# Kernel tuning notes

Hardware: AMD Instinct MI355X
Metric: run time of the kernel (lower is better)

The kernel has to match this reference:

```python
import jax, jax.numpy as jnp
import numpy as np


def _lstm_dir(xs, Wih, Whh, bih, bhh, reverse):
    # xs: [T, B, E]; torch LSTM gate order i, f, g, o
    B = xs.shape[1]
    H = Whh.shape[1]
    h0 = jnp.zeros((B, H), xs.dtype)
    c0 = jnp.zeros((B, H), xs.dtype)

    def step(carry, xt):
        h, c = carry
        g = xt @ Wih.T + h @ Whh.T + (bih + bhh)
        i, f, gg, o = jnp.split(g, 4, axis=-1)
        i = jax.nn.sigmoid(i)
        f = jax.nn.sigmoid(f)
        gg = jnp.tanh(gg)
        o = jax.nn.sigmoid(o)
        c_new = f * c + i * gg
        h_new = o * jnp.tanh(c_new)
        return (h_new, c_new), h_new

    _, hs = jax.lax.scan(step, (h0, c0), xs, reverse=reverse)
    return hs  # [T, B, H] time-aligned


def _forward(x, edge_index, emb_table, Wih_f, Whh_f, bih_f, bhh_f,
             Wih_b, Whh_b, bih_b, bhh_b, label_emb, ggc_weight,
             gru_Wih, gru_Whh, gru_bih, gru_bhh, proj_W, proj_b):
    # --- embedding (dropout is identity in eval) ---
    emb = emb_table[x]                       # [B, T, E]
    xs = jnp.transpose(emb, (1, 0, 2))       # [T, B, E]
    hf = _lstm_dir(xs, Wih_f, Whh_f, bih_f, bhh_f, reverse=False)
    hb = _lstm_dir(xs, Wih_b, Whh_b, bih_b, bhh_b, reverse=True)
    c = jnp.concatenate([hf, hb], axis=-1)   # [T, B, 2H]
    c = jnp.transpose(c, (1, 0, 2))          # [B, T, 2H]

    # --- label cosine similarity, summed over tokens ---
    eps = 1e-8
    cn = c / jnp.maximum(jnp.linalg.norm(c, axis=-1, keepdims=True), eps)
    ln = label_emb / jnp.maximum(jnp.linalg.norm(label_emb, axis=-1, keepdims=True), eps)
    ls = jnp.einsum('btd,ld->bl', cn, ln)    # [B, C] (sum over t folded in)

    # --- GatedGraphConv, 2 layers, aggr='add', edge_weight=None ---
    src, dst = edge_index[0], edge_index[1]
    N = ls.shape[0]
    h = ls
    for i in range(ggc_weight.shape[0]):
        m = h @ ggc_weight[i]                            # [N, C]
        m = jax.ops.segment_sum(m[src], dst, num_segments=N)  # gather + scatter-add
        # torch GRUCell: gates r, z, n
        gi = m @ gru_Wih.T + gru_bih
        gh = h @ gru_Whh.T + gru_bhh
        ir, iz, inn = jnp.split(gi, 3, axis=-1)
        hr, hz, hn = jnp.split(gh, 3, axis=-1)
        r = jax.nn.sigmoid(ir + hr)
        z = jax.nn.sigmoid(iz + hz)
        n = jnp.tanh(inn + r * hn)
        h = (1.0 - z) * n + z * h

    return h @ proj_W.T + proj_b             # [B, C]


def setup_inputs() -> dict:
    key = jax.random.key(0)
    ks = jax.random.split(key, 20)
    V, E, B, T, C, NE = 50000, 300, 2048, 64, 1024, 65536
    H = E
    s = 0.05
    inp = {
        'x': jax.random.randint(ks[0], (B, T), 0, V),
        'edge_index': jax.random.randint(ks[1], (2, NE), 0, B),
        'emb_table': jax.random.normal(ks[2], (V, E)) * s,
        'Wih_f': jax.random.normal(ks[3], (4 * H, E)) * s,
        'Whh_f': jax.random.normal(ks[4], (4 * H, H)) * s,
        'bih_f': jnp.zeros((4 * H,)),
        'bhh_f': jnp.zeros((4 * H,)),
        'Wih_b': jax.random.normal(ks[5], (4 * H, E)) * s,
        'Whh_b': jax.random.normal(ks[6], (4 * H, H)) * s,
        'bih_b': jnp.zeros((4 * H,)),
        'bhh_b': jnp.zeros((4 * H,)),
        'label_emb': jax.random.normal(ks[7], (C, 2 * H)) * s,
        'ggc_weight': jax.random.normal(ks[8], (2, C, C)) * (1.0 / np.sqrt(C)),
        'gru_Wih': jax.random.normal(ks[9], (3 * C, C)) * (1.0 / np.sqrt(C)),
        'gru_Whh': jax.random.normal(ks[10], (3 * C, C)) * (1.0 / np.sqrt(C)),
        'gru_bih': jnp.zeros((3 * C,)),
        'gru_bhh': jnp.zeros((3 * C,)),
        'proj_W': jax.random.normal(ks[11], (C, C)) * (1.0 / np.sqrt(C)),
        'proj_b': jnp.zeros((C,)),
    }
    return inp


def reference(x, edge_index, emb_table, Wih_f, Whh_f, bih_f, bhh_f,
              Wih_b, Whh_b, bih_b, bhh_b, label_emb, ggc_weight,
              gru_Wih, gru_Whh, gru_bih, gru_bhh, proj_W, proj_b):
    return _forward(x, edge_index, emb_table, Wih_f, Whh_f, bih_f, bhh_f,
                    Wih_b, Whh_b, bih_b, bhh_b, label_emb, ggc_weight,
                    gru_Wih, gru_Whh, gru_bih, gru_bhh, proj_W, proj_b)
```

## Files before the change

### kernel.cpp

```cpp
#include <hip/hip_runtime.h>
#include <hip/hip_bf16.h>
#include <stdint.h>

typedef __hip_bfloat16 bf16;
typedef __attribute__((ext_vector_type(8))) short frag16;
typedef __attribute__((ext_vector_type(4))) float f32x4;

#define B_ 2048
#define T_ 64
#define E_ 300
#define H_ 300
#define C_ 1024
#define V_ 50000
#define NE_ 65536
#define HP 320
#define KC 640
#define NP 1280

static __device__ __forceinline__ float sigf(float x) {
  x = fminf(fmaxf(x, -30.f), 30.f);
  return 1.f / (1.f + __expf(-x));
}
static __device__ __forceinline__ float tanhfast(float x) {
  x = fminf(fmaxf(x, -15.f), 15.f);
  float e = __expf(2.f * x);
  return (e - 1.f) / (e + 1.f);
}
static __device__ __forceinline__ float ldraw(const void* p, size_t i, int isb) {
  return isb ? __bfloat162float(((const bf16*)p)[i]) : ((const float*)p)[i];
}
static __device__ __forceinline__ short b2s(bf16 b) {
  short s; __builtin_memcpy(&s, &b, 2); return s;
}
static __device__ __forceinline__ short4 f4tob4(float4 v) {
  return make_short4(b2s(__float2bfloat16(v.x)), b2s(__float2bfloat16(v.y)),
                     b2s(__float2bfloat16(v.z)), b2s(__float2bfloat16(v.w)));
}

static __device__ __forceinline__ void g2l16(const void* g, void* l) {
  __builtin_amdgcn_global_load_lds(
      (const __attribute__((address_space(1))) void*)(uintptr_t)g,
      (__attribute__((address_space(3))) void*)(uintptr_t)l, 16, 0, 0);
}

__global__ void detect_dtype(const unsigned short* __restrict__ e2, int* __restrict__ flag) {
  __shared__ int red[4];
  int tid = threadIdx.x;
  int ones = 0;
#pragma unroll
  for (int s = 0; s < 16; ++s) ones += (e2[2 * (tid * 16 + s)] >> 14) & 1;
  for (int off = 32; off > 0; off >>= 1) ones += __shfl_down(ones, off, 64);
  if ((tid & 63) == 0) red[tid >> 6] = ones;
  __syncthreads();
  if (tid == 0) {
    int tot = red[0] + red[1] + red[2] + red[3];
    *flag = (tot < 1024) ? 1 : 0;
  }
}

__global__ __launch_bounds__(256) void gemm_bt(
    const bf16* A, int lda, const bf16* W, int ldw, const float* bias,
    float* Cf, bf16* Cb, int ldc, int K,
    const int* __restrict__ rawp, int outmode,
    const bf16* A2, const bf16* W2, const float* bias2, float* Cf2) {
  if (blockIdx.z) { A = A2; W = W2; bias = bias2; Cf = Cf2; Cb = nullptr; }
  __shared__ __align__(16) short As[128 * 32];
  __shared__ __align__(16) short Bs[128 * 32];
  const int isb = rawp ? *rawp : 1;
  const int n0 = blockIdx.x * 128, m0 = blockIdx.y * 128;
  const int lane = threadIdx.x & 63, wv = threadIdx.x >> 6;
  const int wm = (wv & 1) * 64, wn = (wv >> 1) * 64;
  const int gr = lane >> 2;
  const int gc = (lane & 3) * 8;
  const short* pA0 = (const short*)A + (size_t)(m0 + wv * 32 + gr) * lda + gc;
  const short* pA1 = pA0 + (size_t)16 * lda;
  const short* pB0 = (const short*)W + (size_t)(n0 + wv * 32 + gr) * ldw + gc;
  const short* pB1 = pB0 + (size_t)16 * ldw;
  short* lA = As + wv * 1024;
  short* lB = Bs + wv * 1024;

  f32x4 acc[4][4];
#pragma unroll
  for (int i = 0; i < 4; ++i)
#pragma unroll
    for (int j = 0; j < 4; ++j) acc[i][j] = (f32x4){0.f, 0.f, 0.f, 0.f};

  const int krd = (lane >> 4) * 8;
  const int rsel = lane & 15;
  for (int k0 = 0; k0 < K; k0 += 32) {
    g2l16(pA0 + k0, lA);
    g2l16(pA1 + k0, lA + 512);
    g2l16(pB0 + k0, lB);
    g2l16(pB1 + k0, lB + 512);
    __syncthreads();
    frag16 af[4], bfg[4];
#pragma unroll
    for (int i = 0; i < 4; ++i) af[i] = *(const frag16*)&As[(wm + i * 16 + rsel) * 32 + krd];
#pragma unroll
    for (int i = 0; i < 4; ++i) bfg[i] = *(const frag16*)&Bs[(wn + i * 16 + rsel) * 32 + krd];
#pragma unroll
    for (int i = 0; i < 4; ++i)
#pragma unroll
      for (int j = 0; j < 4; ++j)
        acc[i][j] = __builtin_amdgcn_mfma_f32_16x16x32_bf16(af[i], bfg[j], acc[i][j], 0, 0, 0);
    __syncthreads();
  }
  const int rq = (lane >> 4) * 4, cq = lane & 15;
#pragma unroll
  for (int j = 0; j < 4; ++j) {
    int cidx = n0 + wn + j * 16 + cq;
    float bv = bias ? bias[cidx] : 0.f;
#pragma unroll
    for (int i = 0; i < 4; ++i) {
      int rbase = m0 + wm + i * 16 + rq;
#pragma unroll
      for (int r = 0; r < 4; ++r) {
        float v = acc[i][j][r] + bv;
        size_t idx = (size_t)(rbase + r) * ldc + cidx;
        if (outmode) {
          if (isb) Cb[idx] = __float2bfloat16(v);
          else Cf[idx] = v;
        } else {
          if (Cf) Cf[idx] = v;
          if (Cb) Cb[idx] = __float2bfloat16(v);
        }
      }
    }
  }
}

static __device__ __forceinline__ void normacc_row2(
    const bf16* hfA, const bf16* hbA, const bf16* hfB, const bf16* hbB,
    float* __restrict__ Spf, int b, int lane) {
  float vA[10], vB[10];
  float sA = 0.f, sB = 0.f;
#pragma unroll
  for (int s = 0; s < 10; ++s) {
    int d = lane + 64 * s;
    float a = 0.f, c = 0.f;
    if (d < 300) {
      a = __bfloat162float(hfA[d]);
      c = __bfloat162float(hfB[d]);
    } else if (d < 600) {
      a = __bfloat162float(hbA[d - 300]);
      c = __bfloat162float(hbB[d - 300]);
    }
    vA[s] = a; vB[s] = c;
    sA += a * a; sB += c * c;
  }
#pragma unroll
  for (int off = 32; off > 0; off >>= 1) {
    sA += __shfl_xor(sA, off, 64);
    sB += __shfl_xor(sB, off, 64);
  }
  float kA = 1.f / fmaxf(sqrtf(sA), 1e-8f);
  float kB = 1.f / fmaxf(sqrtf(sB), 1e-8f);
  float* dst = Spf + (size_t)b * KC;
#pragma unroll
  for (int s = 0; s < 10; ++s) {
    int d = lane + 64 * s;
    if (d < 600) dst[d] += vA[s] * kA + vB[s] * kB;
  }
}

__global__ __launch_bounds__(256) void lstm_step(
    const void* __restrict__ emb, const bf16* __restrict__ embtail,
    const int* __restrict__ x,
    const bf16* __restrict__ Wcat, const float* __restrict__ bcat,
    bf16* __restrict__ hpad, float* __restrict__ cstate,
    bf16* __restrict__ Hfst, bf16* __restrict__ Hbst, float* __restrict__ Spf,
    int s, const int* __restrict__ flagp) {
  const int pb = s & 1;
  const int lane = threadIdx.x & 63, wv = threadIdx.x >> 6;

  if (blockIdx.z == 2) {
    if (s >= 33) {
      int bid = blockIdx.x + gridDim.x * blockIdx.y;
      const bf16* hinf = hpad + (size_t)pb * B_ * HP;
      const bf16* hinb = hpad + (size_t)(2 + pb) * B_ * HP;
      const int t1 = s - 1, t2 = 64 - s;
#pragma unroll
      for (int rep = 0; rep < 2; ++rep) {
        int b = bid * 4 + wv + 1280 * rep;
        if (b < B_)
          normacc_row2(hinf + (size_t)b * HP,
                       Hbst + ((size_t)(t1 - 32) * B_ + b) * H_,
                       Hfst + ((size_t)t2 * B_ + b) * H_,
                       hinb + (size_t)b * HP, Spf, b, lane);
      }
    }
    return;
  }

  __shared__ __align__(16) char smem[16384];
  short* As = (short*)smem;
  short* Bs = (short*)(smem + 4096);
  float* epi = (float*)smem;

  const int dir = blockIdx.z;
  const int tt = dir ? (T_ - 1 - s) : s;
  const int isb = *flagp;
  const bf16* hin = hpad + (size_t)(dir * 2 + pb) * B_ * HP;
  const bf16* Wd = Wcat + (size_t)dir * NP * KC;
  bf16* hout = hpad + (size_t)(dir * 2 + (1 - pb)) * B_ * HP;
  float* cs = cstate + (size_t)dir * B_ * HP;
  const int n0 = blockIdx.x * 128, m0 = blockIdx.y * 64;
  const int wm = (wv & 1) * 32, wn = (wv >> 1) * 64;
  const int gr = lane >> 2;
  const int gc = (lane & 3) * 8;
  const int arow = m0 + wv * 16 + gr;
  const int tok = x[arow * T_ + tt];
  const short* es = (const short*)emb;
  const float* ef = (const float*)emb;
  const short* px = es + (size_t)tok * E_ + gc;
  const short* ptail = (const short*)embtail + (size_t)tok * 32 + gc;
  const short* ph = (const short*)hin + (size_t)arow * HP + gc;
  const short* pB0 = (const short*)Wd + (size_t)(n0 + wv * 32 + gr) * KC + gc;
  const short* pB1 = pB0 + (size_t)16 * KC;
  short* lA = As + wv * 512;
  short* lB = Bs + wv * 1024;

  f32x4 acc[2][4];
#pragma unroll
  for (int i = 0; i < 2; ++i)
#pragma unroll
    for (int j = 0; j < 4; ++j) acc[i][j] = (f32x4){0.f, 0.f, 0.f, 0.f};

  const int rsel = lane & 15, krd = (lane >> 4) * 8;
  for (int kk = 0; kk < KC / 32; ++kk) {
    const int k0 = kk * 32;
    if (k0 < HP) {
      if (isb) {
        g2l16(k0 == 288 ? ptail : (px + k0), lA);
      } else {
        int c0 = k0 + gc;
        float4 fa = (c0 < E_) ? *(const float4*)(ef + (size_t)tok * E_ + c0)
                              : make_float4(0.f, 0.f, 0.f, 0.f);
        float4 fb = (c0 + 4 < E_) ? *(const float4*)(ef + (size_t)tok * E_ + c0 + 4)
                                  : make_float4(0.f, 0.f, 0.f, 0.f);
        short* d = As + (wv * 16 + gr) * 32 + gc;
        *(short4*)d = f4tob4(fa);
        *(short4*)(d + 4) = f4tob4(fb);
      }
    } else {
      g2l16(ph + (k0 - HP), lA);
    }
    g2l16(pB0 + k0, lB);
    g2l16(pB1 + k0, lB + 512);
    __syncthreads();
    frag16 af[2], bfg[4];
#pragma unroll
    for (int i = 0; i < 2; ++i) af[i] = *(const frag16*)&As[(wm + i * 16 + rsel) * 32 + krd];
#pragma unroll
    for (int j = 0; j < 4; ++j) bfg[j] = *(const frag16*)&Bs[(wn + j * 16 + rsel) * 32 + krd];
#pragma unroll
    for (int i = 0; i < 2; ++i)
#pragma unroll
      for (int j = 0; j < 4; ++j)
        acc[i][j] = __builtin_amdgcn_mfma_f32_16x16x32_bf16(af[i], bfg[j], acc[i][j], 0, 0, 0);
    __syncthreads();
  }

  const int rq = (lane >> 4) * 4, cq = lane & 15;
#pragma unroll
  for (int p = 0; p < 2; ++p) {
    if (wn == p * 64) {
#pragma unroll
      for (int j = 0; j < 4; ++j) {
        int cl = j * 16 + cq;
        float bv = bcat[dir * NP + n0 + p * 64 + cl];
#pragma unroll
        for (int i = 0; i < 2; ++i) {
          int rl = wm + i * 16 + rq;
#pragma unroll
          for (int r = 0; r < 4; ++r) epi[(rl + r) * 64 + cl] = acc[i][j][r] + bv;
        }
      }
    }
    __syncthreads();
    int jbase = (n0 + p * 64) >> 2;
    for (int it = threadIdx.x; it < 64 * 16; it += 256) {
      int rl = it >> 4, jl = it & 15;
      int jg = jbase + jl;
      if (jg < H_) {
        const float* row = epi + rl * 64 + jl * 4;
        float iv = sigf(row[0]);
        float fv = sigf(row[1]);
        float gv = tanhfast(row[2]);
        float ov = sigf(row[3]);
        int b = m0 + rl;
        float c = fv * cs[(size_t)b * HP + jg] + iv * gv;
        float h = ov * tanhfast(c);
        cs[(size_t)b * HP + jg] = c;
        bf16 hb = __float2bfloat16(h);
        hout[(size_t)b * HP + jg] = hb;
        if (dir) {
          if (tt >= 32) Hbst[((size_t)(tt - 32) * B_ + b) * H_ + jg] = hb;
        } else if (tt < 32) {
          Hfst[((size_t)tt * B_ + b) * H_ + jg] = hb;
        }
      }
    }
    __syncthreads();
  }
}

__global__ __launch_bounds__(256) void normacc_fin(const bf16* __restrict__ hpad,
                                                   const bf16* __restrict__ Hfst,
                                                   const bf16* __restrict__ Hbst,
                                                   float* __restrict__ Spf) {
  int b = blockIdx.x * 4 + (threadIdx.x >> 6);
  int lane = threadIdx.x & 63;
  normacc_row2(hpad + (size_t)b * HP,
               Hbst + ((size_t)31 * B_ + b) * H_,
               Hfst + (size_t)b * H_,
               hpad + (size_t)2 * B_ * HP + (size_t)b * HP, Spf, b, lane);
}

__global__ void prep_all(const void* __restrict__ Wih_f, const void* __restrict__ Whh_f,
                         const void* __restrict__ bih_f, const void* __restrict__ bhh_f,
                         const void* __restrict__ Wih_b, const void* __restrict__ Whh_b,
                         const void* __restrict__ bih_b, const void* __restrict__ bhh_b,
                         const void* __restrict__ label, const void* __restrict__ ggcw,
                         const void* __restrict__ emb,
                         bf16* __restrict__ Wcat, float* __restrict__ bcat,
                         bf16* __restrict__ lnp, bf16* __restrict__ ggct,
                         bf16* __restrict__ embtail,
                         const int* __restrict__ flagp) {
  const int isb = *flagp;
  if (blockIdx.x < 1024) {
    int l = blockIdx.x, tid = threadIdx.x;
    __shared__ float red[4];
    float v[3];
    float ss = 0.f;
#pragma unroll
    for (int s = 0; s < 3; ++s) {
      int d = tid + 256 * s;
      v[s] = (d < 600) ? ldraw(label, (size_t)l * 600 + d, isb) : 0.f;
      ss += v[s] * v[s];
    }
    for (int off = 32; off > 0; off >>= 1) ss += __shfl_down(ss, off, 64);
    if ((tid & 63) == 0) red[tid >> 6] = ss;
    __syncthreads();
    float scale = 1.f / fmaxf(sqrtf(red[0] + red[1] + red[2] + red[3]), 1e-8f);
#pragma unroll
    for (int s = 0; s < 3; ++s) {
      int d = tid + 256 * s;
      if (d < KC) lnp[(size_t)l * KC + d] = __float2bfloat16(v[s] * scale);
    }
    return;
  }
  int i = (blockIdx.x - 1024) * 256 + threadIdx.x;
  if (i < 2 * NP * KC) {
    int k = i % KC;
    int n = (i / KC) % NP;
    int dir = i / (KC * NP);
    int j = n >> 2, q = n & 3;
    const void* Wih = dir ? Wih_b : Wih_f;
    const void* Whh = dir ? Whh_b : Whh_f;
    float v = 0.f;
    if (j < H_) {
      int row = q * H_ + j;
      if (k < E_) v = ldraw(Wih, (size_t)row * E_ + k, isb);
      else if (k >= HP && k < HP + H_) v = ldraw(Whh, (size_t)row * H_ + (k - HP), isb);
    }
    Wcat[i] = __float2bfloat16(v);
    if (k == 0) {
      const void* bih = dir ? bih_b : bih_f;
      const void* bhh = dir ? bhh_b : bhh_f;
      bcat[dir * NP + n] =
          (j < H_) ? (ldraw(bih, q * H_ + j, isb) + ldraw(bhh, q * H_ + j, isb)) : 0.f;
    }
    return;
  }
  i -= 2 * NP * KC;
  if (i < 2 * C_ * C_) {
    int k = i & 1023, n = (i >> 10) & 1023, l = i >> 20;
    size_t src = ((size_t)l << 20) | ((size_t)k << 10) | (size_t)n;
    ggct[i] = __float2bfloat16(ldraw(ggcw, src, isb));
    return;
  }
  i -= 2 * C_ * C_;
  if (i < V_ * 32) {
    int v = i >> 5, c = i & 31;
    float val = (c < E_ - 288) ? ldraw(emb, (size_t)v * E_ + 288 + c, isb) : 0.f;
    embtail[i] = __float2bfloat16(val);
  }
}

__global__ void prep2(const void* __restrict__ gWih, const void* __restrict__ gWhh,
                      const void* __restrict__ projW, const void* __restrict__ gbih,
                      const void* __restrict__ gbhh, const void* __restrict__ projb,
                      bf16* __restrict__ gWihb, bf16* __restrict__ gWhhb,
                      bf16* __restrict__ projWb, float* __restrict__ gbihf,
                      float* __restrict__ gbhhf, float* __restrict__ projbf,
                      const int* __restrict__ flagp) {
  const int isb = *flagp;
  int i = blockIdx.x * 256 + threadIdx.x;
  if (i < 3072 * C_) { gWihb[i] = __float2bfloat16(ldraw(gWih, i, isb)); return; }
  i -= 3072 * C_;
  if (i < 3072 * C_) { gWhhb[i] = __float2bfloat16(ldraw(gWhh, i, isb)); return; }
  i -= 3072 * C_;
  if (i < C_ * C_) { projWb[i] = __float2bfloat16(ldraw(projW, i, isb)); return; }
  i -= C_ * C_;
  if (i < 3072) { gbihf[i] = ldraw(gbih, i, isb); return; }
  i -= 3072;
  if (i < 3072) { gbhhf[i] = ldraw(gbhh, i, isb); return; }
  i -= 3072;
  if (i < C_) { projbf[i] = ldraw(projb, i, isb); }
}

__global__ void zero_u4(uint4* __restrict__ p, int n16) {
  int i = blockIdx.x * 256 + threadIdx.x;
  if (i < n16) p[i] = make_uint4(0u, 0u, 0u, 0u);
}

__global__ void edge_cnt(const int* __restrict__ ei, int* __restrict__ cnt) {
  int e = blockIdx.x * 256 + threadIdx.x;
  if (e < NE_) {
    int s = ei[e], d = ei[NE_ + e];
    atomicAdd(&cnt[(size_t)d * B_ + s], 1);
  }
}
__global__ void cnt2bf(const int* __restrict__ cnt, bf16* __restrict__ A) {
  int i = blockIdx.x * 256 + threadIdx.x;
  A[i] = __float2bfloat16((float)cnt[i]);
}

__global__ void gru_ew(const float* __restrict__ gi, const float* __restrict__ gh,
                       float* __restrict__ h, bf16* __restrict__ hb16) {
  int i = blockIdx.x * 256 + threadIdx.x;
  int b = i >> 10, j = i & 1023;
  const float* gib = gi + (size_t)b * 3072;
  const float* ghb = gh + (size_t)b * 3072;
  float r = sigf(gib[j] + ghb[j]);
  float z = sigf(gib[1024 + j] + ghb[1024 + j]);
  float n = tanhfast(gib[2048 + j] + r * ghb[2048 + j]);
  float hv = (1.f - z) * n + z * h[i];
  h[i] = hv;
  hb16[i] = __float2bfloat16(hv);
}

__global__ void spcvt(const float* __restrict__ Spf, bf16* __restrict__ Sp) {
  int i = blockIdx.x * 256 + threadIdx.x;
  Sp[i] = __float2bfloat16(Spf[i]);
}

__global__ void sentinel(bf16* __restrict__ o, int n, float v) {
  int i = blockIdx.x * 256 + threadIdx.x;
  if (i < n) o[i] = __float2bfloat16(v);
}

extern "C" void kernel_launch(void* const* d_in, const int* in_sizes, int n_in,
                              void* d_out, int out_size, void* d_ws, size_t ws_size,
                              hipStream_t stream) {
  const int* x = (const int*)d_in[0];
  const int* ei = (const int*)d_in[1];
  const void* emb = d_in[2];
  const void* Wih_f = d_in[3];
  const void* Whh_f = d_in[4];
  const void* bih_f = d_in[5];
  const void* bhh_f = d_in[6];
  const void* Wih_b = d_in[7];
  const void* Whh_b = d_in[8];
  const void* bih_b = d_in[9];
  const void* bhh_b = d_in[10];
  const void* label = d_in[11];
  const void* ggcw = d_in[12];
  const void* gWih = d_in[13];
  const void* gWhh = d_in[14];
  const void* gbih = d_in[15];
  const void* gbhh = d_in[16];
  const void* projW = d_in[17];
  const void* projb = d_in[18];
  (void)in_sizes; (void)n_in;

  const size_t NEED = (size_t)112 * 1024 * 1024;
  if (ws_size < NEED) {
    float v = 100.f + (float)(ws_size >> 24);
    sentinel<<<(out_size + 255) / 256, 256, 0, stream>>>((bf16*)d_out, out_size, v);
    return;
  }

  char* w = (char*)d_ws;
  size_t off = 0;
  auto alloc = [&](size_t bytes) {
    char* p = w + off;
    off += (bytes + 255) & ~(size_t)255;
    return p;
  };
  int* dflag = (int*)alloc(256);
  bf16* Wcat = (bf16*)alloc((size_t)2 * NP * KC * 2);
  float* bcat = (float*)alloc((size_t)2 * NP * 4);
  bf16* lnp = (bf16*)alloc((size_t)C_ * KC * 2);
  bf16* ggct = (bf16*)alloc((size_t)2 * C_ * C_ * 2);
  bf16* Sp = (bf16*)alloc((size_t)B_ * KC * 2);
  bf16* embtail = (bf16*)alloc((size_t)V_ * 32 * 2);
  const size_t phase_base = off;
  float* Spf = (float*)alloc((size_t)B_ * KC * 4);
  bf16* hpad = (bf16*)alloc((size_t)4 * B_ * HP * 2);
  float* cst = (float*)alloc((size_t)2 * B_ * HP * 4);
  bf16* Hfst = (bf16*)alloc((size_t)32 * B_ * H_ * 2);
  bf16* Hbst = (bf16*)alloc((size_t)32 * B_ * H_ * 2);
  off = phase_base;
  float* hbuf = (float*)alloc((size_t)B_ * C_ * 4);
  bf16* hb16 = (bf16*)alloc((size_t)B_ * C_ * 2);
  bf16* m1t = (bf16*)alloc((size_t)C_ * B_ * 2);
  bf16* aggb = (bf16*)alloc((size_t)B_ * C_ * 2);
  bf16* Acnt = (bf16*)alloc((size_t)B_ * B_ * 2);
  float* gi = (float*)alloc((size_t)B_ * 3072 * 4);
  float* gh = (float*)alloc((size_t)B_ * 3072 * 4);
  bf16* gWihb = (bf16*)alloc((size_t)3072 * C_ * 2);
  bf16* gWhhb = (bf16*)alloc((size_t)3072 * C_ * 2);
  bf16* projWb = (bf16*)alloc((size_t)C_ * C_ * 2);
  float* gbihf = (float*)alloc(3072 * 4);
  float* gbhhf = (float*)alloc(3072 * 4);
  float* projbf = (float*)alloc(C_ * 4);
  int* cnt = (int*)gi;

  detect_dtype<<<1, 256, 0, stream>>>((const unsigned short*)emb, dflag);
  prep_all<<<1024 + (2 * NP * KC + 2 * C_ * C_ + V_ * 32) / 256, 256, 0, stream>>>(
      Wih_f, Whh_f, bih_f, bhh_f, Wih_b, Whh_b, bih_b, bhh_b, label, ggcw, emb,
      Wcat, bcat, lnp, ggct, embtail, dflag);
  zero_u4<<<(3 * 327680) / 256, 256, 0, stream>>>((uint4*)Spf, 3 * 327680);

  for (int s = 0; s < T_; ++s)
    lstm_step<<<dim3(NP / 128, B_ / 64, 3), 256, 0, stream>>>(emb, embtail, x, Wcat, bcat,
                                                              hpad, cst, Hfst, Hbst, Spf,
                                                              s, dflag);
  normacc_fin<<<B_ / 4, 256, 0, stream>>>(hpad, Hfst, Hbst, Spf);
  spcvt<<<(B_ * KC) / 256, 256, 0, stream>>>(Spf, Sp);

  prep2<<<(2 * 3072 * C_ + C_ * C_ + 2 * 3072 + C_) / 256, 256, 0, stream>>>(
      gWih, gWhh, projW, gbih, gbhh, projb, gWihb, gWhhb, projWb, gbihf, gbhhf, projbf, dflag);

  gemm_bt<<<dim3(C_ / 128, B_ / 128), 256, 0, stream>>>(Sp, KC, lnp, KC, nullptr,
                                                        hbuf, hb16, C_, KC, nullptr, 0,
                                                        nullptr, nullptr, nullptr, nullptr);
  zero_u4<<<(B_ * B_ * 4 / 16) / 256, 256, 0, stream>>>((uint4*)cnt, B_ * B_ * 4 / 16);
  edge_cnt<<<NE_ / 256, 256, 0, stream>>>(ei, cnt);
  cnt2bf<<<(B_ * B_) / 256, 256, 0, stream>>>(cnt, Acnt);
  for (int l = 0; l < 2; ++l) {
    gemm_bt<<<dim3(B_ / 128, C_ / 128), 256, 0, stream>>>(ggct + (size_t)l * C_ * C_, C_,
                                                          hb16, C_, nullptr,
                                                          nullptr, m1t, B_, C_, nullptr, 0,
                                                          nullptr, nullptr, nullptr, nullptr);
    gemm_bt<<<dim3(C_ / 128, B_ / 128), 256, 0, stream>>>(Acnt, B_, m1t, B_, nullptr,
                                                          nullptr, aggb, C_, B_, nullptr, 0,
                                                          nullptr, nullptr, nullptr, nullptr);
    gemm_bt<<<dim3(3072 / 128, B_ / 128, 2), 256, 0, stream>>>(aggb, C_, gWihb, C_, gbihf,
                                                               gi, nullptr, 3072, C_, nullptr, 0,
                                                               hb16, gWhhb, gbhhf, gh);
    gru_ew<<<(B_ * C_) / 256, 256, 0, stream>>>(gi, gh, hbuf, hb16);
  }
  gemm_bt<<<dim3(C_ / 128, B_ / 128), 256, 0, stream>>>(hb16, C_, projWb, C_, projbf,
                                                        (float*)d_out, (bf16*)d_out, C_, C_,
                                                        dflag, 1,
                                                        nullptr, nullptr, nullptr, nullptr);
}
```

Before: 2.271 ms.

## Double-buffer LDS tiles with async prefetch in GEMM and LSTM step kernels

Converts the single-buffered global-to-LDS tile loads in the generic GEMM and the per-timestep LSTM kernel into a two-stage ping-pong pipeline. The next K tile is issued before computing the current one, with explicit vmcnt waits and raw barriers in place of __syncthreads. This is meant to hide global load latency behind MFMA work. It costs extra shared memory, which may lower occupancy, and relies on hand-counted vmcnt values that must match the number of outstanding loads.

Result: faster. 2.226 ms (-2.0%).

```diff
diff --git a/kernel.cpp b/kernel.cpp
--- a/kernel.cpp
+++ b/kernel.cpp
@@ -64,8 +64,8 @@
     const int* __restrict__ rawp, int outmode,
     const bf16* A2, const bf16* W2, const float* bias2, float* Cf2) {
   if (blockIdx.z) { A = A2; W = W2; bias = bias2; Cf = Cf2; Cb = nullptr; }
-  __shared__ __align__(16) short As[128 * 32];
-  __shared__ __align__(16) short Bs[128 * 32];
+  __shared__ __align__(16) short As[2][128 * 32];
+  __shared__ __align__(16) short Bs[2][128 * 32];
   const int isb = rawp ? *rawp : 1;
   const int n0 = blockIdx.x * 128, m0 = blockIdx.y * 128;
   const int lane = threadIdx.x & 63, wv = threadIdx.x >> 6;
@@ -76,8 +76,15 @@
   const short* pA1 = pA0 + (size_t)16 * lda;
   const short* pB0 = (const short*)W + (size_t)(n0 + wv * 32 + gr) * ldw + gc;
   const short* pB1 = pB0 + (size_t)16 * ldw;
-  short* lA = As + wv * 1024;
-  short* lB = Bs + wv * 1024;
+
+  auto issueT = [&](int k0, int buf) {
+    short* a = &As[buf][wv * 1024];
+    short* b = &Bs[buf][wv * 1024];
+    g2l16(pA0 + k0, a);
+    g2l16(pA1 + k0, a + 512);
+    g2l16(pB0 + k0, b);
+    g2l16(pB1 + k0, b + 512);
+  };
 
   f32x4 acc[4][4];
 #pragma unroll
@@ -85,25 +92,29 @@
 #pragma unroll
     for (int j = 0; j < 4; ++j) acc[i][j] = (f32x4){0.f, 0.f, 0.f, 0.f};
 
+  const int nk = K / 32;
   const int krd = (lane >> 4) * 8;
   const int rsel = lane & 15;
-  for (int k0 = 0; k0 < K; k0 += 32) {
-    g2l16(pA0 + k0, lA);
-    g2l16(pA1 + k0, lA + 512);
-    g2l16(pB0 + k0, lB);
-    g2l16(pB1 + k0, lB + 512);
-    __syncthreads();
+  issueT(0, 0);
+  if (nk > 1) issueT(32, 1);
+  for (int kk = 0; kk < nk; ++kk) {
+    const int cur = kk & 1;
+    if (kk + 1 < nk) asm volatile("s_waitcnt vmcnt(4)" ::: "memory");
+    else asm volatile("s_waitcnt vmcnt(0)" ::: "memory");
+    __builtin_amdgcn_s_barrier();
     frag16 af[4], bfg[4];
 #pragma unroll
-    for (int i = 0; i < 4; ++i) af[i] = *(const frag16*)&As[(wm + i * 16 + rsel) * 32 + krd];
-#pragma unroll
-    for (int i = 0; i < 4; ++i) bfg[i] = *(const frag16*)&Bs[(wn + i * 16 + rsel) * 32 + krd];
+    for (int i = 0; i < 4; ++i) af[i] = *(const frag16*)&As[cur][(wm + i * 16 + rsel) * 32 + krd];
+#pragma unroll
+    for (int i = 0; i < 4; ++i) bfg[i] = *(const frag16*)&Bs[cur][(wn + i * 16 + rsel) * 32 + krd];
 #pragma unroll
     for (int i = 0; i < 4; ++i)
 #pragma unroll
       for (int j = 0; j < 4; ++j)
         acc[i][j] = __builtin_amdgcn_mfma_f32_16x16x32_bf16(af[i], bfg[j], acc[i][j], 0, 0, 0);
-    __syncthreads();
+    asm volatile("" ::: "memory");
+    __builtin_amdgcn_s_barrier();
+    if (kk + 2 < nk) issueT(32 * (kk + 2), cur);
   }
   const int rq = (lane >> 4) * 4, cq = lane & 15;
 #pragma unroll
@@ -192,9 +203,11 @@
     return;
   }
 
-  __shared__ __align__(16) char smem[16384];
-  short* As = (short*)smem;
-  short* Bs = (short*)(smem + 4096);
+  __shared__ __align__(16) char smem[24576];
+  short* As0 = (short*)smem;
+  short* As1 = (short*)(smem + 4096);
+  short* Bs0 = (short*)(smem + 8192);
+  short* Bs1 = (short*)(smem + 16384);
   float* epi = (float*)smem;
 
   const int dir = blockIdx.z;
@@ -217,8 +230,18 @@
   const short* ph = (const short*)hin + (size_t)arow * HP + gc;
   const short* pB0 = (const short*)Wd + (size_t)(n0 + wv * 32 + gr) * KC + gc;
   const short* pB1 = pB0 + (size_t)16 * KC;
-  short* lA = As + wv * 512;
-  short* lB = Bs + wv * 1024;
+
+  auto issueT = [&](int k0, int buf) {
+    short* a = (buf ? As1 : As0) + wv * 512;
+    short* b = (buf ? Bs1 : Bs0) + wv * 1024;
+    if (k0 < HP) {
+      g2l16(k0 == 288 ? ptail : (px + k0), a);
+    } else {
+      g2l16(ph + (k0 - HP), a);
+    }
+    g2l16(pB0 + k0, b);
+    g2l16(pB1 + k0, b + 512);
+  };
 
   f32x4 acc[2][4];
 #pragma unroll
@@ -227,38 +250,55 @@
     for (int j = 0; j < 4; ++j) acc[i][j] = (f32x4){0.f, 0.f, 0.f, 0.f};
 
   const int rsel = lane & 15, krd = (lane >> 4) * 8;
-  for (int kk = 0; kk < KC / 32; ++kk) {
-    const int k0 = kk * 32;
-    if (k0 < HP) {
-      if (isb) {
-        g2l16(k0 == 288 ? ptail : (px + k0), lA);
-      } else {
+  const int NKT = KC / 32;
+
+  auto mfma8 = [&](const short* Ap, const short* Bp) {
+    frag16 af[2], bfg[4];
+#pragma unroll
+    for (int i = 0; i < 2; ++i) af[i] = *(const frag16*)&Ap[(wm + i * 16 + rsel) * 32 + krd];
+#pragma unroll
+    for (int j = 0; j < 4; ++j) bfg[j] = *(const frag16*)&Bp[(wn + j * 16 + rsel) * 32 + krd];
+#pragma unroll
+    for (int i = 0; i < 2; ++i)
+#pragma unroll
+      for (int j = 0; j < 4; ++j)
+        acc[i][j] = __builtin_amdgcn_mfma_f32_16x16x32_bf16(af[i], bfg[j], acc[i][j], 0, 0, 0);
+  };
+
+  if (isb) {
+    issueT(0, 0);
+    issueT(32, 1);
+    for (int kk = 0; kk < NKT; ++kk) {
+      const int cur = kk & 1;
+      if (kk + 1 < NKT) asm volatile("s_waitcnt vmcnt(3)" ::: "memory");
+      else asm volatile("s_waitcnt vmcnt(0)" ::: "memory");
+      __builtin_amdgcn_s_barrier();
+      mfma8(cur ? As1 : As0, cur ? Bs1 : Bs0);
+      asm volatile("" ::: "memory");
+      __builtin_amdgcn_s_barrier();
+      if (kk + 2 < NKT) issueT(32 * (kk + 2), cur);
+    }
+  } else {
+    for (int kk = 0; kk < NKT; ++kk) {
+      const int k0 = kk * 32;
+      if (k0 < HP) {
         int c0 = k0 + gc;
         float4 fa = (c0 < E_) ? *(const float4*)(ef + (size_t)tok * E_ + c0)
                               : make_float4(0.f, 0.f, 0.f, 0.f);
         float4 fb = (c0 + 4 < E_) ? *(const float4*)(ef + (size_t)tok * E_ + c0 + 4)
                                   : make_float4(0.f, 0.f, 0.f, 0.f);
-        short* d = As + (wv * 16 + gr) * 32 + gc;
+        short* d = As0 + (wv * 16 + gr) * 32 + gc;
         *(short4*)d = f4tob4(fa);
         *(short4*)(d + 4) = f4tob4(fb);
+      } else {
+        g2l16(ph + (k0 - HP), As0 + wv * 512);
       }
-    } else {
-      g2l16(ph + (k0 - HP), lA);
-    }
-    g2l16(pB0 + k0, lB);
-    g2l16(pB1 + k0, lB + 512);
-    __syncthreads();
-    frag16 af[2], bfg[4];
-#pragma unroll
-    for (int i = 0; i < 2; ++i) af[i] = *(const frag16*)&As[(wm + i * 16 + rsel) * 32 + krd];
-#pragma unroll
-    for (int j = 0; j < 4; ++j) bfg[j] = *(const frag16*)&Bs[(wn + j * 16 + rsel) * 32 + krd];
-#pragma unroll
-    for (int i = 0; i < 2; ++i)
-#pragma unroll
-      for (int j = 0; j < 4; ++j)
-        acc[i][j] = __builtin_amdgcn_mfma_f32_16x16x32_bf16(af[i], bfg[j], acc[i][j], 0, 0, 0);
-    __syncthreads();
+      g2l16(pB0 + k0, Bs0 + wv * 1024);
+      g2l16(pB1 + k0, Bs0 + wv * 1024 + 512);
+      __syncthreads();
+      mfma8(As0, Bs0);
+      __syncthreads();
+    }
   }
 
   const int rq = (lane >> 4) * 4, cq = lane & 15;
```
